# Kernel tuning notes

Hardware: AMD Instinct MI355X
Metric: run time of the kernel (lower is better)

Reference implementation:

```python
import jax, jax.numpy as jnp
import numpy as np

VOCAB = 128
NUM_PATHS = 100     # num_paths sampled from the lattice
NBEST_SCALE = 0.5   # scale on scores before sampling (k2.random_paths)
TEMPERATURE = 1.0   # logprob temperature before normalization
BLANK = 0           # CTC blank token


def setup_inputs() -> dict:
    key = jax.random.key(0)
    k1, k2, k3, k4 = jax.random.split(key, 4)
    B, T, L = 8, 500, 100
    logits = jax.random.normal(k1, (B, T, VOCAB), jnp.float32)
    emissions = jax.nn.log_softmax(logits, -1)  # acoustic-model log-probs (N, T, C)
    emissions_lengths = jax.random.randint(k2, (B,), 400, T + 1).astype(jnp.int32)
    labels = jax.random.randint(k3, (B, L), 1, VOCAB).astype(jnp.int32)
    labels_length = jax.random.randint(k4, (B,), 80, L + 1).astype(jnp.int32)
    return {"emissions": emissions, "emissions_lengths": emissions_lengths,
            "labels": labels, "labels_length": labels_length}


def _mwer(emissions, emissions_lengths, labels, labels_length):
    B, T, V = emissions.shape
    L = labels.shape[1]
    P = NUM_PATHS
    key = jax.random.key(1)
    # --- N-best path sampling: Gumbel perturbation of nbest_scale-scaled log-probs ---
    u = jax.random.uniform(key, (B, P, T, V), emissions.dtype, 1e-6, 1.0 - 1e-6)
    g = -jnp.log(-jnp.log(u))
    tokens = jnp.argmax(emissions[:, None] * NBEST_SCALE + g, axis=-1)  # (B, P, T)
    frame_mask = jnp.arange(T)[None, None, :] < emissions_lengths[:, None, None]
    # path log-prob under the model (unscaled scores), temperature-scaled
    lp = jnp.take_along_axis(emissions[:, None], tokens[..., None], axis=-1)[..., 0]
    path_logp = jnp.sum(jnp.where(frame_mask, lp, 0.0), axis=-1) / TEMPERATURE  # (B, P)
    # --- CTC collapse (ctc_topo semantics: drop blanks + repeats) into padded hyps ---
    prev = jnp.concatenate([jnp.full_like(tokens[..., :1], -1), tokens[..., :-1]], -1)
    keep = (tokens != BLANK) & (tokens != prev) & frame_mask
    pos = jnp.where(keep, jnp.cumsum(keep, -1) - 1, T)  # dropped frames -> dump slot T
    BP = B * P
    tok2, pos2 = tokens.reshape(BP, T), pos.reshape(BP, T)
    hyp = jnp.full((BP, T + 1), -1, tokens.dtype).at[jnp.arange(BP)[:, None], pos2].set(tok2)[:, :T]
    hyp_len = keep.reshape(BP, T).sum(-1)
    # --- Levenshtein alignment: exact edit distance hyp vs ref (vectorized DP) ---
    refs = jnp.repeat(labels, P, axis=0)             # (BP, L)  hyp_to_ref_map
    ref_len = jnp.repeat(labels_length, P, axis=0)   # (BP,)
    dp0 = jnp.broadcast_to(jnp.arange(L + 1, dtype=jnp.int32), (BP, L + 1))
    js = jnp.arange(L + 1, dtype=jnp.int32)[None, :]

    def step(dp, x):
        h, valid = x  # hyp token (BP,), valid flag (BP,)
        cost = (refs != h[:, None]).astype(jnp.int32)                       # (BP, L)
        cand = jnp.concatenate([dp[:, :1] + 1,
                                jnp.minimum(dp[:, 1:] + 1, dp[:, :-1] + cost)], 1)
        # insertion chain new[j] = min(cand[j], new[j-1]+1) via min-plus prefix
        new = jax.lax.cummin(cand - js, axis=1) + js
        return jnp.where(valid[:, None], new, dp), None

    valid = jnp.arange(T)[:, None] < hyp_len[None, :]  # (T, BP)
    dp, _ = jax.lax.scan(step, dp0, (hyp.T, valid))
    wers = jnp.take_along_axis(dp, ref_len[:, None], 1)[:, 0].reshape(B, P)
    wers = jax.lax.stop_gradient(wers.astype(emissions.dtype))
    # --- MWER: normalize path posteriors per utterance, expected WER, 'mean' ---
    prob = jax.nn.softmax(path_logp, axis=1)
    return jnp.mean(prob * wers)


def reference(emissions, emissions_lengths, labels, labels_length):
    return _mwer(emissions, emissions_lengths, labels, labels_length)
```

## Files before the change

### kernel.cpp

```cpp
#include <hip/hip_runtime.h>
#include <stdint.h>

#define NB 8
#define NP 100
#define NT 500
#define NV 128
#define NBP 800
#define TS 512
#define ES 500
#define NITEMS (NB * NT * 50)

typedef unsigned long long u64;

#define ROTL(x, r) __builtin_amdgcn_alignbit((x), (x), 32 - (r))

__device__ __forceinline__ uint32_t threefry01_lo(uint32_t x0, uint32_t x1) {
  const uint32_t k0 = 0u, k1 = 1u;
  const uint32_t k2 = 0x1BD11BDAu ^ k0 ^ k1;
  x0 += k0; x1 += k1;
#define TF_R(r) { x0 += x1; x1 = ROTL(x1, r); x1 ^= x0; }
  TF_R(13) TF_R(15) TF_R(26) TF_R(6)
  x0 += k1; x1 += k2 + 1u;
  TF_R(17) TF_R(29) TF_R(16) TF_R(24)
  x0 += k2; x1 += k0 + 2u;
  TF_R(13) TF_R(15) TF_R(26) TF_R(6)
  x0 += k0; x1 += k1 + 3u;
  TF_R(17) TF_R(29) TF_R(16) TF_R(24)
  x0 += k1; x1 += k2 + 4u;
  TF_R(13) TF_R(15) TF_R(26) TF_R(6)
  x1 += k0 + 5u;
#undef TF_R
  return x1;
}

__global__ __launch_bounds__(256) void k_sample(
    const float* __restrict__ em, const int* __restrict__ elen,
    uint8_t* __restrict__ tok2, float* __restrict__ lp2t, int item_base) {
  __shared__ float snw[3][NV + 1];
  const int tid = threadIdx.x;
  const int i0 = item_base + blockIdx.x * 64;
  const int R0 = i0 / 50;
  for (int i = tid; i < 3 * NV; i += 256) {
    const int r = i >> 7, v = i & 127;
    int R = R0 + r; R = R < NB * NT ? R : NB * NT - 1;
    snw[r][v] = -__builtin_amdgcn_exp2f(em[(size_t)R * NV + v] * -0.7213475204444817f);
  }
  __syncthreads();
  const int item = i0 + (tid >> 2);
  const int q = tid & 3;
  if (item >= NITEMS) return;
  const int R = item / 50;
  const int pp = item - R * 50;
  const int b = R / NT;
  const int t = R - b * NT;
  if (t >= elen[b]) return;
  const int r = R - R0;
  const int vh = q << 5;
  const int bp0 = b * NP + 2 * pp;
  const uint32_t base0 = ((uint32_t)(bp0 * NT + t) << 7) + (uint32_t)vh;
  const uint32_t base1 = base0 + (uint32_t)(NT << 7);
  const float span = (float)(1.0 - 1e-6) - 1e-6f;
  float best0 = 3.0e38f, best1 = 3.0e38f;
  int bi0 = 0, bi1 = 0;
#pragma unroll 8
  for (int i = 0; i < 32; i++) {
    const uint32_t r0 = threefry01_lo(0u, base0 + (uint32_t)i);
    const uint32_t r1 = threefry01_lo(0u, base1 + (uint32_t)i);
    const float f0 = __uint_as_float((r0 >> 9) | 0x3f800000u) - 1.0f;
    const float f1 = __uint_as_float((r1 >> 9) | 0x3f800000u) - 1.0f;
    const float u0 = fmaf(f0, span, 1e-6f);
    const float u1 = fmaf(f1, span, 1e-6f);
    const float w = snw[r][vh + i];
    const float s0 = __log2f(u0) * w;
    const float s1 = __log2f(u1) * w;
    if (s0 < best0) { best0 = s0; bi0 = vh + i; }
    if (s1 < best1) { best1 = s1; bi1 = vh + i; }
  }
#pragma unroll
  for (int off = 1; off <= 2; off <<= 1) {
    const float oa = __shfl_xor(best0, off); const int ia = __shfl_xor(bi0, off);
    if (oa < best0 || (oa == best0 && ia < bi0)) { best0 = oa; bi0 = ia; }
    const float ob = __shfl_xor(best1, off); const int ib = __shfl_xor(bi1, off);
    if (ob < best1 || (ob == best1 && ib < bi1)) { best1 = ob; bi1 = ib; }
  }
  if (q == 0) {
    const float e0 = em[(size_t)R * NV + bi0];
    const float e1 = em[(size_t)R * NV + bi1];
    tok2[(size_t)bp0 * TS + t] = (uint8_t)bi0;
    tok2[(size_t)(bp0 + 1) * TS + t] = (uint8_t)bi1;
    *(float2*)&lp2t[(size_t)t * NBP + bp0] = make_float2(e0, e1);
  }
}

__global__ __launch_bounds__(128) void k_pq(
    const int* __restrict__ labels, const int* __restrict__ llen,
    uint4* __restrict__ pqg) {
  const int b = blockIdx.x;
  const int c = threadIdx.x;
  const int m = llen[b];
  const int* __restrict__ lab = labels + b * 100;
  uint32_t a0 = 0, a1 = 0, a2 = 0, a3 = 0;
  const int e0 = m < 32 ? m : 32, e1 = m < 64 ? m : 64;
  const int e2 = m < 96 ? m : 96, e3 = m;
  for (int i = 0; i < e0; i++)  a0 |= (uint32_t)(lab[i] == c) << i;
  for (int i = 32; i < e1; i++) a1 |= (uint32_t)(lab[i] == c) << (i - 32);
  for (int i = 64; i < e2; i++) a2 |= (uint32_t)(lab[i] == c) << (i - 64);
  for (int i = 96; i < e3; i++) a3 |= (uint32_t)(lab[i] == c) << (i - 96);
  pqg[b * NV + c] = make_uint4(a0, a1, a2, a3);
}

__global__ __launch_bounds__(64) void k_ce(
    const uint8_t* __restrict__ tok2, const uint4* __restrict__ pqg,
    const int* __restrict__ elen, uint4* __restrict__ eqc,
    int* __restrict__ nkept) {
  __shared__ uint4 pqs[NV];
  const int bp = blockIdx.x;
  const int b = bp / NP;
  const int lane = threadIdx.x;
  pqs[lane] = pqg[b * NV + lane];
  pqs[lane + 64] = pqg[b * NV + lane + 64];
  __syncthreads();
  const int el = elen[b];
  const uint8_t* __restrict__ row = tok2 + (size_t)bp * TS;
  uint4* __restrict__ orow = eqc + (size_t)bp * ES;
  int off = 0;
  for (int t0 = 0; t0 < el; t0 += 64) {
    const int t = t0 + lane;
    const bool inb = (t < el);
    const int c = inb ? row[t] : 0;
    const int cp = (t == 0) ? 255 : (inb ? row[t - 1] : 255);
    const bool kept = inb && (c != 0) && (c != cp);
    const u64 mask = __ballot(kept);
    const int idx = off + (int)__builtin_amdgcn_mbcnt_hi(
        (uint32_t)(mask >> 32),
        __builtin_amdgcn_mbcnt_lo((uint32_t)mask, 0u));
    if (kept) orow[idx] = pqs[c];
    off += (int)__popcll(mask);
  }
  if (lane == 0) nkept[bp] = off;
}

__device__ __forceinline__ void loadg(uint4 (&B)[4], int g, const uint4* __restrict__ rowp) {
#pragma unroll
  for (int i = 0; i < 4; i++) {
    int t = g * 4 + i;
    t = t < ES ? t : ES - 1;
    B[i] = rowp[t];
  }
}

__device__ __forceinline__ void procg(const uint4 (&B)[4], int fbase, int nk,
                                      u64 hmask,
                                      u64& Pv0, u64& Pv1, u64& Mv0, u64& Mv1,
                                      int& score) {
#pragma unroll
  for (int i = 0; i < 4; i++) {
    if (fbase + i >= nk) break;
    const u64 Eq0 = (u64)B[i].x | ((u64)B[i].y << 32);
    const u64 Eq1 = (u64)B[i].z | ((u64)B[i].w << 32);
    const u64 Xv0 = Eq0 | Mv0, Xv1 = Eq1 | Mv1;
    const u64 EP0 = Eq0 & Pv0, EP1 = Eq1 & Pv1;
    const u64 sA = EP0 + Pv0;
    const u64 sB = EP1 + Pv1 + (sA < EP0 ? 1ull : 0ull);
    const u64 Xh0 = (sA ^ Pv0) | Eq0;
    const u64 Xh1 = (sB ^ Pv1) | Eq1;
    const u64 Ph0 = Mv0 | ~(Xh0 | Pv0);
    const u64 Ph1 = Mv1 | ~(Xh1 | Pv1);
    const u64 Mh0 = Pv0 & Xh0, Mh1 = Pv1 & Xh1;
    score += (int)((Ph1 & hmask) != 0) - (int)((Mh1 & hmask) != 0);
    const u64 nPh1 = (Ph1 << 1) | (Ph0 >> 63);
    const u64 nPh0 = (Ph0 << 1) | 1ull;
    const u64 nMh1 = (Mh1 << 1) | (Mh0 >> 63);
    const u64 nMh0 = (Mh0 << 1);
    Pv0 = nMh0 | ~(Xv0 | nPh0);
    Pv1 = nMh1 | ~(Xv1 | nPh1);
    Mv0 = nPh0 & Xv0;
    Mv1 = nPh1 & Xv1;
  }
}

__global__ __launch_bounds__(64) void k_dp(
    const uint4* __restrict__ eqc, const int* __restrict__ nkept,
    const int* __restrict__ llen, float* __restrict__ wer) {
  const int b = blockIdx.x, h = blockIdx.y;
  const int tid = threadIdx.x;
  const bool active = (tid < 50);
  const int bp = b * NP + h * 50 + (active ? tid : 49);
  const int m = llen[b];
  const int nk = nkept[bp];
  const uint4* __restrict__ rowp = eqc + (size_t)bp * ES;
  u64 Pv0 = ~0ull, Pv1 = ~0ull, Mv0 = 0ull, Mv1 = 0ull;
  int score = m;
  const u64 hmask = 1ull << ((m - 1) & 63);

  const int ngl = (nk + 3) >> 2;
  int ngmax = ngl;
  for (int off = 1; off < 64; off <<= 1) {
    const int o = __shfl_xor(ngmax, off);
    ngmax = o > ngmax ? o : ngmax;
  }
  uint4 B0[4], B1[4], B2[4], B3[4];
  loadg(B0, 0, rowp); loadg(B1, 1, rowp);
  loadg(B2, 2, rowp); loadg(B3, 3, rowp);
  int g = 0;
  while (g + 4 <= ngmax) {
    procg(B0, (g    ) * 4, nk, hmask, Pv0, Pv1, Mv0, Mv1, score);
    loadg(B0, g + 4, rowp);
    procg(B1, (g + 1) * 4, nk, hmask, Pv0, Pv1, Mv0, Mv1, score);
    loadg(B1, g + 5, rowp);
    procg(B2, (g + 2) * 4, nk, hmask, Pv0, Pv1, Mv0, Mv1, score);
    loadg(B2, g + 6, rowp);
    procg(B3, (g + 3) * 4, nk, hmask, Pv0, Pv1, Mv0, Mv1, score);
    loadg(B3, g + 7, rowp);
    g += 4;
  }
  if (g     < ngmax) procg(B0, (g    ) * 4, nk, hmask, Pv0, Pv1, Mv0, Mv1, score);
  if (g + 1 < ngmax) procg(B1, (g + 1) * 4, nk, hmask, Pv0, Pv1, Mv0, Mv1, score);
  if (g + 2 < ngmax) procg(B2, (g + 2) * 4, nk, hmask, Pv0, Pv1, Mv0, Mv1, score);
  if (active) wer[bp] = (float)score;
}

__global__ __launch_bounds__(128) void k_red(
    const float* __restrict__ lp2t, const int* __restrict__ elen,
    double* __restrict__ pred) {
  const int b = blockIdx.x, k = blockIdx.y;
  const int tid = threadIdx.x;
  const bool active = (tid < NP);
  const int p = active ? tid : NP - 1;
  const int el = elen[b];
  const int t0 = k * 125;
  const int t1 = (t0 + 125 < el) ? t0 + 125 : el;
  const float* __restrict__ col = lp2t + b * NP + p;
  double s = 0.0;
#pragma unroll 8
  for (int t = t0; t < t1; t++) s += (double)col[(size_t)t * NBP];
  if (active) pred[(size_t)(b * NP + p) * 4 + k] = s;
}

__global__ __launch_bounds__(512) void k_fin(
    const double* __restrict__ pred, const float* __restrict__ wer,
    float* __restrict__ out) {
  __shared__ float partial[NB];
  const int w = threadIdx.x >> 6, lane = threadIdx.x & 63;
  const int base = w * NP;
  float l0 = -1e30f, l1 = -1e30f;
  if (lane < NP) {
    const double* pr = pred + (size_t)(base + lane) * 4;
    l0 = (float)(pr[0] + pr[1] + pr[2] + pr[3]);
  }
  if (lane + 64 < NP) {
    const double* pr = pred + (size_t)(base + lane + 64) * 4;
    l1 = (float)(pr[0] + pr[1] + pr[2] + pr[3]);
  }
  float mx = fmaxf(l0, l1);
  for (int off = 1; off < 64; off <<= 1) mx = fmaxf(mx, __shfl_xor(mx, off));
  const float e0 = (lane < NP) ? __expf(l0 - mx) : 0.0f;
  const float e1 = (lane + 64 < NP) ? __expf(l1 - mx) : 0.0f;
  const float w0 = (lane < NP) ? wer[base + lane] : 0.0f;
  const float w1 = (lane + 64 < NP) ? wer[base + lane + 64] : 0.0f;
  float s = e0 + e1;
  float a = e0 * w0 + e1 * w1;
  for (int off = 1; off < 64; off <<= 1) {
    s += __shfl_xor(s, off);
    a += __shfl_xor(a, off);
  }
  if (lane == 0) partial[w] = a / s;
  __syncthreads();
  if (threadIdx.x == 0) {
    float tot = 0.0f;
    for (int i = 0; i < NB; i++) tot += partial[i];
    out[0] = tot * (1.0f / (float)NBP);
  }
}

extern "C" void kernel_launch(void* const* d_in, const int* in_sizes, int n_in,
                              void* d_out, int out_size, void* d_ws, size_t ws_size,
                              hipStream_t stream) {
  const float* em     = (const float*)d_in[0];
  const int*   elen   = (const int*)d_in[1];
  const int*   labels = (const int*)d_in[2];
  const int*   llen   = (const int*)d_in[3];
  float* out = (float*)d_out;
  char* ws = (char*)d_ws;
  uint4*   eqc   = (uint4*)ws;
  uint8_t* tok2  = (uint8_t*)(ws + 6400000);
  float*   lp2t  = (float*)(ws + 6809600);
  float*   wer   = (float*)(ws + 8409600);
  double*  pred  = (double*)(ws + 8412800);
  int*     nkept = (int*)(ws + 8438400);
  uint4*   pqg   = (uint4*)(ws + 8441600);

  k_sample<<<dim3(1563), dim3(256), 0, stream>>>(em, elen, tok2, lp2t, 0);
  k_sample<<<dim3(1562), dim3(256), 0, stream>>>(em, elen, tok2, lp2t, 1563 * 64);
  k_pq<<<dim3(NB), dim3(128), 0, stream>>>(labels, llen, pqg);
  k_ce<<<dim3(NBP), dim3(64), 0, stream>>>(tok2, pqg, elen, eqc, nkept);
  k_dp<<<dim3(NB, 2), dim3(64), 0, stream>>>(eqc, nkept, llen, wer);
  k_red<<<dim3(NB, 4), dim3(128), 0, stream>>>(lp2t, elen, pred);
  k_fin<<<dim3(1), dim3(512), 0, stream>>>(pred, wer, out);
}
```

Measured before the change: 199.6 us.

## Process four paths per sampler thread and interleave two paths per DP thread

The sampling kernel now has each 4-lane group handle four path samples per frame instead of two. This halves the block count, merges the two launches into one, and writes a float4 of log-probs. The bit-parallel edit-distance kernel now runs two independent paths per thread in 8 blocks instead of 16, interleaving their dependency chains to hide latency. This trades parallelism for more instruction-level parallelism: fewer waves occupy the GPU, and register pressure rises in both kernels.

```diff
diff --git a/kernel.cpp b/kernel.cpp
--- a/kernel.cpp
+++ b/kernel.cpp
@@ -8,7 +8,7 @@
 #define NBP 800
 #define TS 512
 #define ES 500
-#define NITEMS (NB * NT * 50)
+#define PAIRS (NB * NT * 25)
 
 typedef unsigned long long u64;
 
@@ -35,60 +35,79 @@
 
 __global__ __launch_bounds__(256) void k_sample(
     const float* __restrict__ em, const int* __restrict__ elen,
-    uint8_t* __restrict__ tok2, float* __restrict__ lp2t, int item_base) {
-  __shared__ float snw[3][NV + 1];
+    uint8_t* __restrict__ tok2, float* __restrict__ lp2t) {
+  __shared__ float snw[4][NV + 1];
   const int tid = threadIdx.x;
-  const int i0 = item_base + blockIdx.x * 64;
-  const int R0 = i0 / 50;
-  for (int i = tid; i < 3 * NV; i += 256) {
+  const int pi0 = blockIdx.x * 64;
+  const int R0 = pi0 / 25;
+  for (int i = tid; i < 4 * NV; i += 256) {
     const int r = i >> 7, v = i & 127;
     int R = R0 + r; R = R < NB * NT ? R : NB * NT - 1;
     snw[r][v] = -__builtin_amdgcn_exp2f(em[(size_t)R * NV + v] * -0.7213475204444817f);
   }
   __syncthreads();
-  const int item = i0 + (tid >> 2);
-  const int q = tid & 3;
-  if (item >= NITEMS) return;
-  const int R = item / 50;
-  const int pp = item - R * 50;
+  const int gg = blockIdx.x * 256 + tid;
+  const int pitem = gg >> 2, q = gg & 3;
+  if (pitem >= PAIRS) return;
+  const int R = pitem / 25;
+  const int pp = pitem - R * 25;
   const int b = R / NT;
   const int t = R - b * NT;
   if (t >= elen[b]) return;
   const int r = R - R0;
   const int vh = q << 5;
-  const int bp0 = b * NP + 2 * pp;
-  const uint32_t base0 = ((uint32_t)(bp0 * NT + t) << 7) + (uint32_t)vh;
-  const uint32_t base1 = base0 + (uint32_t)(NT << 7);
+  const int bp0 = b * NP + 4 * pp;
+  const uint32_t baseA = ((uint32_t)(bp0 * NT + t) << 7) + (uint32_t)vh;
+  const uint32_t baseB = baseA + (uint32_t)(NT << 7);
+  const uint32_t baseC = baseB + (uint32_t)(NT << 7);
+  const uint32_t baseD = baseC + (uint32_t)(NT << 7);
   const float span = (float)(1.0 - 1e-6) - 1e-6f;
-  float best0 = 3.0e38f, best1 = 3.0e38f;
-  int bi0 = 0, bi1 = 0;
+  float bvA = 3.0e38f, bvB = 3.0e38f, bvC = 3.0e38f, bvD = 3.0e38f;
+  int biA = 0, biB = 0, biC = 0, biD = 0;
 #pragma unroll 8
   for (int i = 0; i < 32; i++) {
-    const uint32_t r0 = threefry01_lo(0u, base0 + (uint32_t)i);
-    const uint32_t r1 = threefry01_lo(0u, base1 + (uint32_t)i);
-    const float f0 = __uint_as_float((r0 >> 9) | 0x3f800000u) - 1.0f;
-    const float f1 = __uint_as_float((r1 >> 9) | 0x3f800000u) - 1.0f;
-    const float u0 = fmaf(f0, span, 1e-6f);
-    const float u1 = fmaf(f1, span, 1e-6f);
+    const uint32_t rA = threefry01_lo(0u, baseA + (uint32_t)i);
+    const uint32_t rB = threefry01_lo(0u, baseB + (uint32_t)i);
+    const uint32_t rC = threefry01_lo(0u, baseC + (uint32_t)i);
+    const uint32_t rD = threefry01_lo(0u, baseD + (uint32_t)i);
     const float w = snw[r][vh + i];
-    const float s0 = __log2f(u0) * w;
-    const float s1 = __log2f(u1) * w;
-    if (s0 < best0) { best0 = s0; bi0 = vh + i; }
-    if (s1 < best1) { best1 = s1; bi1 = vh + i; }
+    const float fA = __uint_as_float((rA >> 9) | 0x3f800000u) - 1.0f;
+    const float fB = __uint_as_float((rB >> 9) | 0x3f800000u) - 1.0f;
+    const float fC = __uint_as_float((rC >> 9) | 0x3f800000u) - 1.0f;
+    const float fD = __uint_as_float((rD >> 9) | 0x3f800000u) - 1.0f;
+    const float uA = fmaf(fA, span, 1e-6f);
+    const float uB = fmaf(fB, span, 1e-6f);
+    const float uC = fmaf(fC, span, 1e-6f);
+    const float uD = fmaf(fD, span, 1e-6f);
+    const float sA = __log2f(uA) * w;
+    const float sB = __log2f(uB) * w;
+    const float sC = __log2f(uC) * w;
+    const float sD = __log2f(uD) * w;
+    if (sA < bvA) { bvA = sA; biA = vh + i; }
+    if (sB < bvB) { bvB = sB; biB = vh + i; }
+    if (sC < bvC) { bvC = sC; biC = vh + i; }
+    if (sD < bvD) { bvD = sD; biD = vh + i; }
   }
 #pragma unroll
   for (int off = 1; off <= 2; off <<= 1) {
-    const float oa = __shfl_xor(best0, off); const int ia = __shfl_xor(bi0, off);
-    if (oa < best0 || (oa == best0 && ia < bi0)) { best0 = oa; bi0 = ia; }
-    const float ob = __shfl_xor(best1, off); const int ib = __shfl_xor(bi1, off);
-    if (ob < best1 || (ob == best1 && ib < bi1)) { best1 = ob; bi1 = ib; }
+    float ov; int oi;
+    ov = __shfl_xor(bvA, off); oi = __shfl_xor(biA, off);
+    if (ov < bvA || (ov == bvA && oi < biA)) { bvA = ov; biA = oi; }
+    ov = __shfl_xor(bvB, off); oi = __shfl_xor(biB, off);
+    if (ov < bvB || (ov == bvB && oi < biB)) { bvB = ov; biB = oi; }
+    ov = __shfl_xor(bvC, off); oi = __shfl_xor(biC, off);
+    if (ov < bvC || (ov == bvC && oi < biC)) { bvC = ov; biC = oi; }
+    ov = __shfl_xor(bvD, off); oi = __shfl_xor(biD, off);
+    if (ov < bvD || (ov == bvD && oi < biD)) { bvD = ov; biD = oi; }
   }
   if (q == 0) {
-    const float e0 = em[(size_t)R * NV + bi0];
-    const float e1 = em[(size_t)R * NV + bi1];
-    tok2[(size_t)bp0 * TS + t] = (uint8_t)bi0;
-    tok2[(size_t)(bp0 + 1) * TS + t] = (uint8_t)bi1;
-    *(float2*)&lp2t[(size_t)t * NBP + bp0] = make_float2(e0, e1);
+    const float* __restrict__ erow = em + (size_t)R * NV;
+    const float eA = erow[biA], eB = erow[biB], eC = erow[biC], eD = erow[biD];
+    tok2[(size_t)(bp0 + 0) * TS + t] = (uint8_t)biA;
+    tok2[(size_t)(bp0 + 1) * TS + t] = (uint8_t)biB;
+    tok2[(size_t)(bp0 + 2) * TS + t] = (uint8_t)biC;
+    tok2[(size_t)(bp0 + 3) * TS + t] = (uint8_t)biD;
+    *(float4*)&lp2t[(size_t)t * NBP + bp0] = make_float4(eA, eB, eC, eD);
   }
 }
 
@@ -182,42 +201,47 @@
 __global__ __launch_bounds__(64) void k_dp(
     const uint4* __restrict__ eqc, const int* __restrict__ nkept,
     const int* __restrict__ llen, float* __restrict__ wer) {
-  const int b = blockIdx.x, h = blockIdx.y;
+  const int b = blockIdx.x;
   const int tid = threadIdx.x;
   const bool active = (tid < 50);
-  const int bp = b * NP + h * 50 + (active ? tid : 49);
+  const int p0 = b * NP + (active ? tid : 49);
+  const int p1 = p0 + 50;
   const int m = llen[b];
-  const int nk = nkept[bp];
-  const uint4* __restrict__ rowp = eqc + (size_t)bp * ES;
-  u64 Pv0 = ~0ull, Pv1 = ~0ull, Mv0 = 0ull, Mv1 = 0ull;
-  int score = m;
+  const int nk0 = nkept[p0], nk1 = nkept[p1];
+  const uint4* __restrict__ row0 = eqc + (size_t)p0 * ES;
+  const uint4* __restrict__ row1 = eqc + (size_t)p1 * ES;
+  u64 aPv0 = ~0ull, aPv1 = ~0ull, aMv0 = 0ull, aMv1 = 0ull; int as = m;
+  u64 bPv0 = ~0ull, bPv1 = ~0ull, bMv0 = 0ull, bMv1 = 0ull; int bs = m;
   const u64 hmask = 1ull << ((m - 1) & 63);
 
-  const int ngl = (nk + 3) >> 2;
-  int ngmax = ngl;
+  const int ng0 = (nk0 + 3) >> 2, ng1 = (nk1 + 3) >> 2;
+  int ngmax = ng0 > ng1 ? ng0 : ng1;
   for (int off = 1; off < 64; off <<= 1) {
     const int o = __shfl_xor(ngmax, off);
     ngmax = o > ngmax ? o : ngmax;
   }
-  uint4 B0[4], B1[4], B2[4], B3[4];
-  loadg(B0, 0, rowp); loadg(B1, 1, rowp);
-  loadg(B2, 2, rowp); loadg(B3, 3, rowp);
+  uint4 A0[4], A1[4], B0[4], B1[4];
+  loadg(A0, 0, row0); loadg(A1, 0, row1);
+  loadg(B0, 1, row0); loadg(B1, 1, row1);
   int g = 0;
-  while (g + 4 <= ngmax) {
-    procg(B0, (g    ) * 4, nk, hmask, Pv0, Pv1, Mv0, Mv1, score);
-    loadg(B0, g + 4, rowp);
-    procg(B1, (g + 1) * 4, nk, hmask, Pv0, Pv1, Mv0, Mv1, score);
-    loadg(B1, g + 5, rowp);
-    procg(B2, (g + 2) * 4, nk, hmask, Pv0, Pv1, Mv0, Mv1, score);
-    loadg(B2, g + 6, rowp);
-    procg(B3, (g + 3) * 4, nk, hmask, Pv0, Pv1, Mv0, Mv1, score);
-    loadg(B3, g + 7, rowp);
-    g += 4;
-  }
-  if (g     < ngmax) procg(B0, (g    ) * 4, nk, hmask, Pv0, Pv1, Mv0, Mv1, score);
-  if (g + 1 < ngmax) procg(B1, (g + 1) * 4, nk, hmask, Pv0, Pv1, Mv0, Mv1, score);
-  if (g + 2 < ngmax) procg(B2, (g + 2) * 4, nk, hmask, Pv0, Pv1, Mv0, Mv1, score);
-  if (active) wer[bp] = (float)score;
+  while (g + 2 <= ngmax) {
+    procg(A0, g * 4, nk0, hmask, aPv0, aPv1, aMv0, aMv1, as);
+    procg(A1, g * 4, nk1, hmask, bPv0, bPv1, bMv0, bMv1, bs);
+    loadg(A0, g + 2, row0); loadg(A1, g + 2, row1);
+    procg(B0, (g + 1) * 4, nk0, hmask, aPv0, aPv1, aMv0, aMv1, as);
+    procg(B1, (g + 1) * 4, nk1, hmask, bPv0, bPv1, bMv0, bMv1, bs);
+    loadg(B0, g + 3, row0); loadg(B1, g + 3, row1);
+    g += 2;
+  }
+  if (g < ngmax) {
+    procg(A0, g * 4, nk0, hmask, aPv0, aPv1, aMv0, aMv1, as);
+    procg(A1, g * 4, nk1, hmask, bPv0, bPv1, bMv0, bMv1, bs);
+  }
+  if (g + 1 < ngmax) {
+    procg(B0, (g + 1) * 4, nk0, hmask, aPv0, aPv1, aMv0, aMv1, as);
+    procg(B1, (g + 1) * 4, nk1, hmask, bPv0, bPv1, bMv0, bMv1, bs);
+  }
+  if (active) { wer[p0] = (float)as; wer[p1] = (float)bs; }
 }
 
 __global__ __launch_bounds__(128) void k_red(
@@ -290,11 +314,10 @@
   int*     nkept = (int*)(ws + 8438400);
   uint4*   pqg   = (uint4*)(ws + 8441600);
 
-  k_sample<<<dim3(1563), dim3(256), 0, stream>>>(em, elen, tok2, lp2t, 0);
-  k_sample<<<dim3(1562), dim3(256), 0, stream>>>(em, elen, tok2, lp2t, 1563 * 64);
+  k_sample<<<dim3((PAIRS * 4 + 255) / 256), dim3(256), 0, stream>>>(em, elen, tok2, lp2t);
   k_pq<<<dim3(NB), dim3(128), 0, stream>>>(labels, llen, pqg);
   k_ce<<<dim3(NBP), dim3(64), 0, stream>>>(tok2, pqg, elen, eqc, nkept);
-  k_dp<<<dim3(NB, 2), dim3(64), 0, stream>>>(eqc, nkept, llen, wer);
+  k_dp<<<dim3(NB), dim3(64), 0, stream>>>(eqc, nkept, llen, wer);
   k_red<<<dim3(NB, 4), dim3(128), 0, stream>>>(lp2t, elen, pred);
   k_fin<<<dim3(1), dim3(512), 0, stream>>>(pred, wer, out);
 }
```

Measured after the change: 290.3 us. 45.5% more time.
